# Performance work log

Hardware: AMD Instinct MI355X
Metric: run time of the kernel (lower is better)

The kernel has to match this reference:

```python
import jax, jax.numpy as jnp
import numpy as np

WINDOW_SIZE = 32
SIM_THRESHOLD = 0.7
N_TOKENS = 262144
DIM = 256


def setup_inputs() -> dict:
    key = jax.random.key(0)
    x = jax.random.normal(key, (N_TOKENS, DIM), dtype=jnp.float32)
    return {"x": x}


def reference(x):
    """Stage 1 (global window pruning) + Stage 3 (sequential merge) of FocusModules.

    Returns:
      mask1: [N] bool keep-mask equivalent to compute_patch_similarity's index list
             (indices retained are exactly jnp.where(mask1)[0]).
      compressed: [N, D] float, features with stage-3-dropped tokens zeroed
             (mask-compacted form of spatial_token_compression's output; the
             retained rows in order equal the torch output).
    """
    N, D = x.shape
    W = WINDOW_SIZE
    nw = N // W  # N chosen as multiple of W

    # F.normalize(x, p=2, dim=-1) with eps clamp
    norms = jnp.maximum(jnp.linalg.norm(x, axis=-1, keepdims=True), 1e-12)
    xn = x / norms

    # ---- Stage 1: per-window cosine-similarity thresholding (vectorized over windows)
    win = xn.reshape(nw, W, D)
    sim = jnp.einsum('nwd,nvd->nwv', win, win)          # [nw, W, W]
    mean_sim = sim.mean(axis=2)                          # [nw, W]
    mu = mean_sim.mean(axis=1, keepdims=True)
    sd = mean_sim.std(axis=1, ddof=1, keepdims=True)     # torch .std() is unbiased
    keep = ~(mean_sim > (mu + sd))                       # [nw, W] bool
    # fallback: if a window keeps nothing, keep its argmin token
    any_kept = keep.any(axis=1, keepdims=True)
    fallback = jnp.arange(W)[None, :] == mean_sim.argmin(axis=1)[:, None]
    keep = jnp.where(any_kept, keep, fallback)
    mask1 = keep.reshape(N)

    # ---- Stage 3: adjacent-pair cosine similarity pruning
    sim_adj = jnp.sum(xn[:-1] * xn[1:], axis=-1)         # [N-1] (unit vectors -> dot = cosine)
    mask3 = jnp.concatenate([jnp.ones((1,), dtype=bool), sim_adj < SIM_THRESHOLD])
    compressed = x * mask3[:, None].astype(x.dtype)      # zeroed instead of compacted (jit-static shape)

    return mask1, compressed
```

## Files before the change

### kernel.cpp

```cpp
#include <hip/hip_runtime.h>
#include <math.h>

#define TOKW 32
#define DIMS 256
#define F4PT (DIMS / 4)

__global__ __launch_bounds__(256) void focus_kernel(
    const float* __restrict__ x,
    float* __restrict__ out_mask,
    float* __restrict__ out_comp)
{
    const int tid  = threadIdx.x;
    const int lane = tid & 63;
    const int win  = blockIdx.x * 4 + (tid >> 6);

    const long long t0 = (long long)win * TOKW;
    const long long b4 = t0 * F4PT;
    const float4* xv = (const float4*)x;
    float4* ov = (float4*)out_comp;

    float4 row[TOKW];
#pragma unroll
    for (int j = 0; j < TOKW; ++j)
        row[j] = xv[b4 + j * F4PT + lane];

    float4 rp = make_float4(0.f, 0.f, 0.f, 0.f);
    if (win > 0) rp = xv[b4 - F4PT + lane];

    float ssp = rp.x * rp.x + rp.y * rp.y + rp.z * rp.z + rp.w * rp.w;
#pragma unroll
    for (int mm = 1; mm < 64; mm <<= 1) ssp += __shfl_xor(ssp, mm);
    float rn_prev = 1.0f / fmaxf(sqrtf(ssp), 1e-12f);

    float4 s = make_float4(0.f, 0.f, 0.f, 0.f);
    float rn[TOKW];
    unsigned int simbits = 0;

#pragma unroll
    for (int j = 0; j < TOKW; ++j) {
        const float4 rc = row[j];
        const float4 pr = (j == 0) ? rp : row[j - 1];

        float ss = rc.x * rc.x + rc.y * rc.y + rc.z * rc.z + rc.w * rc.w;
        float dd = rc.x * pr.x + rc.y * pr.y + rc.z * pr.z + rc.w * pr.w;
#pragma unroll
        for (int mm = 1; mm < 64; mm <<= 1) {
            ss += __shfl_xor(ss, mm);
            dd += __shfl_xor(dd, mm);
        }
        const float r = 1.0f / fmaxf(sqrtf(ss), 1e-12f);
        rn[j] = r;

        const float sim  = dd * r * rn_prev;
        const float mult = (sim < 0.7f) ? 1.0f : 0.0f;
        if (sim < 0.7f) simbits |= (1u << j);
        (void)simbits;

        ov[b4 + j * F4PT + lane] =
            make_float4(rc.x * mult, rc.y * mult, rc.z * mult, rc.w * mult);

        s.x += rc.x * r; s.y += rc.y * r; s.z += rc.z * r; s.w += rc.w * r;
        rn_prev = r;
    }

    float mlane = 0.f;
#pragma unroll
    for (int j = 0; j < TOKW; ++j) {
        const float4 rc = row[j];
        float dp = rc.x * s.x + rc.y * s.y + rc.z * s.z + rc.w * s.w;
#pragma unroll
        for (int mm = 1; mm < 64; mm <<= 1) dp += __shfl_xor(dp, mm);
        const float mj = dp * rn[j] * (1.0f / 32.0f);
        if (lane == j) mlane = mj;
    }

    float mu = (lane < TOKW) ? mlane : 0.f;
#pragma unroll
    for (int mm = 1; mm < 64; mm <<= 1) mu += __shfl_xor(mu, mm);
    mu *= (1.0f / 32.0f);

    float d = (lane < TOKW) ? (mlane - mu) : 0.f;
    float var = d * d;
#pragma unroll
    for (int mm = 1; mm < 64; mm <<= 1) var += __shfl_xor(var, mm);
    var *= (1.0f / 31.0f);
    const float thr = mu + sqrtf(var);

    const unsigned long long bal =
        __ballot(lane < TOKW && mlane <= thr);
    const int cnt = __popcll(bal);

    float av = (lane < TOKW) ? mlane : 3.402823466e38f;
    int   ai = lane;
#pragma unroll
    for (int mm = 1; mm < 64; mm <<= 1) {
        const float bv = __shfl_xor(av, mm);
        const int   bi = __shfl_xor(ai, mm);
        if (bv < av || (bv == av && bi < ai)) { av = bv; ai = bi; }
    }

    if (lane < TOKW) {
        const bool k = (cnt > 0) ? (mlane <= thr) : (lane == ai);
        out_mask[t0 + lane] = k ? 1.0f : 0.0f;
    }
}

extern "C" void kernel_launch(void* const* d_in, const int* in_sizes, int n_in,
                              void* d_out, int out_size, void* d_ws, size_t ws_size,
                              hipStream_t stream) {
    const float* x = (const float*)d_in[0];
    const int ND = in_sizes[0];
    const int N  = ND / DIMS;
    const int nw = N / TOKW;
    const int nb = nw / 4;

    float* out_mask = (float*)d_out;
    float* out_comp = out_mask + N;

    focus_kernel<<<nb, 256, 0, stream>>>(x, out_mask, out_comp);
}
```

Before: 502.0 us.

## Split each wavefront into 8 token groups with chunked double-buffered loads

Each wavefront now handles 8 tokens at a time, with 8 lanes per token and 8 float4 per lane, in place of all 64 lanes covering one token. Per-token reductions shrink from 6 shuffle stages to 3, and the window is processed in four chunks with two register buffers, reloading chunks for the second pass instead of holding all 32 rows. It also reloads the previous-token rows rather than carrying them along. The aim is to cut shuffle latency and register pressure so occupancy rises, at the cost of reading the input about twice from cache or memory.

```diff
diff --git a/kernel.cpp b/kernel.cpp
--- a/kernel.cpp
+++ b/kernel.cpp
@@ -3,7 +3,33 @@
 
 #define TOKW 32
 #define DIMS 256
-#define F4PT (DIMS / 4)
+#define F4PR 64
+
+typedef float f4 __attribute__((ext_vector_type(4)));
+
+__device__ __forceinline__ float dot4(f4 a, f4 b) {
+    return a[0]*b[0] + a[1]*b[1] + a[2]*b[2] + a[3]*b[3];
+}
+
+__device__ __forceinline__ float bfly124(float v) {
+    v += __shfl_xor(v, 1);
+    v += __shfl_xor(v, 2);
+    v += __shfl_xor(v, 4);
+    return v;
+}
+
+__device__ __forceinline__ f4 shflxor4(f4 v, int m) {
+    f4 r;
+    r[0] = __shfl_xor(v[0], m);
+    r[1] = __shfl_xor(v[1], m);
+    r[2] = __shfl_xor(v[2], m);
+    r[3] = __shfl_xor(v[3], m);
+    return r;
+}
+
+#define KEEP8(a)                                                          \
+    asm volatile("" : "+v"(a[0]), "+v"(a[1]), "+v"(a[2]), "+v"(a[3]),     \
+                      "+v"(a[4]), "+v"(a[5]), "+v"(a[6]), "+v"(a[7]))
 
 __global__ __launch_bounds__(256) void focus_kernel(
     const float* __restrict__ x,
@@ -12,97 +38,155 @@
 {
     const int tid  = threadIdx.x;
     const int lane = tid & 63;
+    const int g    = lane >> 3;
+    const int lt   = lane & 7;
     const int win  = blockIdx.x * 4 + (tid >> 6);
 
-    const long long t0 = (long long)win * TOKW;
-    const long long b4 = t0 * F4PT;
-    const float4* xv = (const float4*)x;
-    float4* ov = (float4*)out_comp;
-
-    float4 row[TOKW];
-#pragma unroll
-    for (int j = 0; j < TOKW; ++j)
-        row[j] = xv[b4 + j * F4PT + lane];
-
-    float4 rp = make_float4(0.f, 0.f, 0.f, 0.f);
-    if (win > 0) rp = xv[b4 - F4PT + lane];
-
-    float ssp = rp.x * rp.x + rp.y * rp.y + rp.z * rp.z + rp.w * rp.w;
-#pragma unroll
-    for (int mm = 1; mm < 64; mm <<= 1) ssp += __shfl_xor(ssp, mm);
-    float rn_prev = 1.0f / fmaxf(sqrtf(ssp), 1e-12f);
-
-    float4 s = make_float4(0.f, 0.f, 0.f, 0.f);
-    float rn[TOKW];
-    unsigned int simbits = 0;
-
-#pragma unroll
-    for (int j = 0; j < TOKW; ++j) {
-        const float4 rc = row[j];
-        const float4 pr = (j == 0) ? rp : row[j - 1];
-
-        float ss = rc.x * rc.x + rc.y * rc.y + rc.z * rc.z + rc.w * rc.w;
-        float dd = rc.x * pr.x + rc.y * pr.y + rc.z * pr.z + rc.w * pr.w;
-#pragma unroll
-        for (int mm = 1; mm < 64; mm <<= 1) {
-            ss += __shfl_xor(ss, mm);
-            dd += __shfl_xor(dd, mm);
-        }
-        const float r = 1.0f / fmaxf(sqrtf(ss), 1e-12f);
-        rn[j] = r;
-
-        const float sim  = dd * r * rn_prev;
-        const float mult = (sim < 0.7f) ? 1.0f : 0.0f;
-        if (sim < 0.7f) simbits |= (1u << j);
-        (void)simbits;
-
-        ov[b4 + j * F4PT + lane] =
-            make_float4(rc.x * mult, rc.y * mult, rc.z * mult, rc.w * mult);
-
-        s.x += rc.x * r; s.y += rc.y * r; s.z += rc.z * r; s.w += rc.w * r;
-        rn_prev = r;
-    }
-
-    float mlane = 0.f;
-#pragma unroll
-    for (int j = 0; j < TOKW; ++j) {
-        const float4 rc = row[j];
-        float dp = rc.x * s.x + rc.y * s.y + rc.z * s.z + rc.w * s.w;
-#pragma unroll
-        for (int mm = 1; mm < 64; mm <<= 1) dp += __shfl_xor(dp, mm);
-        const float mj = dp * rn[j] * (1.0f / 32.0f);
-        if (lane == j) mlane = mj;
-    }
-
-    float mu = (lane < TOKW) ? mlane : 0.f;
-#pragma unroll
-    for (int mm = 1; mm < 64; mm <<= 1) mu += __shfl_xor(mu, mm);
+    const long long t0   = (long long)win * TOKW;
+    const long long base = (t0 + g) * F4PR + lt;
+    const f4* xv = (const f4*)x;
+    f4* ov = (f4*)out_comp;
+
+    const f4 z4 = {0.f, 0.f, 0.f, 0.f};
+
+    f4 vA[8], vB[8], w[8], s[8];
+    float rn_c[4], m_c[4];
+#pragma unroll
+    for (int j = 0; j < 8; ++j) s[j] = z4;
+
+#define LOADV(V, c)                                                       \
+    do {                                                                  \
+        _Pragma("unroll")                                                 \
+        for (int j = 0; j < 8; ++j) V[j] = xv[base + (c)*8*F4PR + 8*j];   \
+        KEEP8(V);                                                         \
+    } while (0)
+
+#define LOADW(c)                                                          \
+    do {                                                                  \
+        const long long tw_ = (t0 + 8*(c) + g - 1) * F4PR + lt;           \
+        _Pragma("unroll")                                                 \
+        for (int j = 0; j < 8; ++j) w[j] = xv[tw_ + 8*j];                 \
+        KEEP8(w);                                                         \
+    } while (0)
+
+#define CHUNK(c, V)                                                       \
+    do {                                                                  \
+        float ss = 0.f, sw = 0.f, dd = 0.f;                               \
+        _Pragma("unroll")                                                 \
+        for (int j = 0; j < 8; ++j) {                                     \
+            ss += dot4(V[j], V[j]);                                       \
+            sw += dot4(w[j], w[j]);                                       \
+            dd += dot4(V[j], w[j]);                                       \
+        }                                                                 \
+        ss = bfly124(ss);                                                 \
+        sw = bfly124(sw);                                                 \
+        dd = bfly124(dd);                                                 \
+        const float r  = 1.0f / fmaxf(sqrtf(ss), 1e-12f);                 \
+        const float rw = 1.0f / fmaxf(sqrtf(sw), 1e-12f);                 \
+        rn_c[c] = r;                                                      \
+        const float mult = (dd * r * rw < 0.7f) ? 1.0f : 0.0f;            \
+        _Pragma("unroll")                                                 \
+        for (int j = 0; j < 8; ++j) {                                     \
+            ov[base + (c)*8*F4PR + 8*j] = V[j] * mult;                    \
+            s[j] += V[j] * r;                                             \
+        }                                                                 \
+    } while (0)
+
+    LOADV(vA, 0);
+    {
+        const long long tp = t0 + g - 1;
+        const bool ok = (tp >= 0);
+        const long long tw_ = (ok ? tp : 0) * F4PR + lt;
+#pragma unroll
+        for (int j = 0; j < 8; ++j) w[j] = ok ? xv[tw_ + 8*j] : z4;
+        KEEP8(w);
+    }
+    LOADV(vB, 1);
+    CHUNK(0, vA);
+    LOADW(1);
+    LOADV(vA, 2);
+    CHUNK(1, vB);
+    LOADW(2);
+    LOADV(vB, 3);
+    CHUNK(2, vA);
+    LOADW(3);
+    LOADV(vA, 0);
+    CHUNK(3, vB);
+    LOADV(vB, 1);
+
+#pragma unroll
+    for (int j = 0; j < 8; ++j) {
+        s[j] += shflxor4(s[j], 8);
+        s[j] += shflxor4(s[j], 16);
+        s[j] += shflxor4(s[j], 32);
+    }
+
+#define MDOT(c, V)                                                        \
+    do {                                                                  \
+        float dp = 0.f;                                                   \
+        _Pragma("unroll")                                                 \
+        for (int j = 0; j < 8; ++j) dp += dot4(V[j], s[j]);               \
+        dp = bfly124(dp);                                                 \
+        m_c[c] = dp * rn_c[c] * (1.0f / 32.0f);                           \
+    } while (0)
+
+    MDOT(0, vA);
+    LOADV(vA, 2);
+    MDOT(1, vB);
+    LOADV(vB, 3);
+    MDOT(2, vA);
+    MDOT(3, vB);
+
+    float mu = m_c[0] + m_c[1] + m_c[2] + m_c[3];
+    mu += __shfl_xor(mu, 8);
+    mu += __shfl_xor(mu, 16);
+    mu += __shfl_xor(mu, 32);
     mu *= (1.0f / 32.0f);
 
-    float d = (lane < TOKW) ? (mlane - mu) : 0.f;
-    float var = d * d;
-#pragma unroll
-    for (int mm = 1; mm < 64; mm <<= 1) var += __shfl_xor(var, mm);
-    var *= (1.0f / 31.0f);
-    const float thr = mu + sqrtf(var);
-
-    const unsigned long long bal =
-        __ballot(lane < TOKW && mlane <= thr);
-    const int cnt = __popcll(bal);
-
-    float av = (lane < TOKW) ? mlane : 3.402823466e38f;
-    int   ai = lane;
-#pragma unroll
-    for (int mm = 1; mm < 64; mm <<= 1) {
+    const float d0 = m_c[0] - mu, d1 = m_c[1] - mu;
+    const float d2 = m_c[2] - mu, d3 = m_c[3] - mu;
+    float vr = d0*d0 + d1*d1 + d2*d2 + d3*d3;
+    vr += __shfl_xor(vr, 8);
+    vr += __shfl_xor(vr, 16);
+    vr += __shfl_xor(vr, 32);
+    vr *= (1.0f / 31.0f);
+    const float thr = mu + sqrtf(vr);
+
+    int cnt = (m_c[0] <= thr) + (m_c[1] <= thr)
+            + (m_c[2] <= thr) + (m_c[3] <= thr);
+    cnt += __shfl_xor(cnt, 8);
+    cnt += __shfl_xor(cnt, 16);
+    cnt += __shfl_xor(cnt, 32);
+
+    float av = m_c[0]; int ai = g;
+    if (m_c[1] < av) { av = m_c[1]; ai = 8 + g; }
+    if (m_c[2] < av) { av = m_c[2]; ai = 16 + g; }
+    if (m_c[3] < av) { av = m_c[3]; ai = 24 + g; }
+#pragma unroll
+    for (int mm = 8; mm <= 32; mm <<= 1) {
         const float bv = __shfl_xor(av, mm);
         const int   bi = __shfl_xor(ai, mm);
         if (bv < av || (bv == av && bi < ai)) { av = bv; ai = bi; }
     }
 
+    const bool anyk = (cnt > 0);
+    const unsigned long long b0 = __ballot(anyk ? (m_c[0] <= thr) : (ai == g));
+    const unsigned long long b1 = __ballot(anyk ? (m_c[1] <= thr) : (ai == 8  + g));
+    const unsigned long long b2 = __ballot(anyk ? (m_c[2] <= thr) : (ai == 16 + g));
+    const unsigned long long b3 = __ballot(anyk ? (m_c[3] <= thr) : (ai == 24 + g));
+
     if (lane < TOKW) {
-        const bool k = (cnt > 0) ? (mlane <= thr) : (lane == ai);
-        out_mask[t0 + lane] = k ? 1.0f : 0.0f;
-    }
+        const unsigned long long bb = (lane < 8)  ? b0
+                                    : (lane < 16) ? b1
+                                    : (lane < 24) ? b2 : b3;
+        const int bit = (int)((bb >> (8 * (lane & 7))) & 1ull);
+        out_mask[t0 + lane] = bit ? 1.0f : 0.0f;
+    }
+
+#undef LOADV
+#undef LOADW
+#undef CHUNK
+#undef MDOT
 }
 
 extern "C" void kernel_launch(void* const* d_in, const int* in_sizes, int n_in,
```

Result: faster. 450.4 us (-10.3%).
